# Optimization experiments

Hardware: AMD Instinct MI355X
Metric: run time of the kernel (lower is better)

The kernel has to match this reference:

```python
import jax, jax.numpy as jnp
import numpy as np

ALPHA = 0.2          # LeakyReLU negative slope
NEG_INF = -9e15      # mask value used by the torch module


def setup_inputs() -> dict:
    key = jax.random.key(0)
    k1, k2, k3, k4 = jax.random.split(key, 4)
    N, F_IN, F_OUT = 8192, 128, 128
    h = jax.random.normal(k1, (N, F_IN), dtype=jnp.float32)
    adj = jax.random.randint(k2, (N, N), 0, 2, dtype=jnp.int32)
    # xavier_uniform(gain=1.414) approximated with scaled normal init
    W = jax.random.normal(k3, (F_IN, F_OUT), dtype=jnp.float32) * (1.414 / np.sqrt(F_IN))
    a = jax.random.normal(k4, (2 * F_OUT, 1), dtype=jnp.float32) * (1.414 / np.sqrt(2 * F_OUT))
    return {"h": h, "adj": adj, "W": W, "a": a}


def reference(h, adj, W, a):
    # Wh: [N, F]
    Wh = h @ W
    F_out = W.shape[1]
    # e[i,j] = LeakyReLU( [Wh_i || Wh_j] . a ) = LeakyReLU( Wh_i.a1 + Wh_j.a2 )
    e_src = Wh @ a[:F_out, 0]   # [N]
    e_dst = Wh @ a[F_out:, 0]   # [N]
    e = jax.nn.leaky_relu(e_src[:, None] + e_dst[None, :], negative_slope=ALPHA)  # [N, N]
    attention = jax.nn.softmax(jnp.where(adj > 0, e, NEG_INF), axis=1)
    # dropout is identity in eval mode
    h_prime = attention @ Wh    # [N, F]
    return h_prime
```

## Files before the change

kernel.cpp:

```cpp
#include <hip/hip_runtime.h>
#include <hip/hip_bf16.h>


#define NN 8192
#define FF 128
#define SEGS 8
#define JSEG (NN / SEGS)
#define NK (JSEG / 32)

typedef __bf16 bf16x8 __attribute__((ext_vector_type(8)));
typedef float floatx4 __attribute__((ext_vector_type(4)));

__device__ __forceinline__ unsigned short f2b(float f) {
    unsigned int u = __float_as_uint(f);
    return (unsigned short)((u + 0x7FFFu + ((u >> 16) & 1u)) >> 16);
}
__device__ __forceinline__ unsigned int pk2(float a, float b) {
    return (unsigned int)f2b(a) | ((unsigned int)f2b(b) << 16);
}

__global__ __launch_bounds__(128) void k0_uv(const float* __restrict__ W,
                                             const float* __restrict__ a,
                                             float* __restrict__ u,
                                             float* __restrict__ v) {
    int k = blockIdx.x, t = threadIdx.x;
    float wv = W[k * FF + t];
    float p1 = wv * a[t];
    float p2 = wv * a[FF + t];
    for (int off = 32; off; off >>= 1) {
        p1 += __shfl_down(p1, off);
        p2 += __shfl_down(p2, off);
    }
    __shared__ float r[4];
    if ((t & 63) == 0) { r[(t >> 6) * 2] = p1; r[(t >> 6) * 2 + 1] = p2; }
    __syncthreads();
    if (t == 0) { u[k] = r[0] + r[2]; v[k] = r[1] + r[3]; }
}

__global__ __launch_bounds__(256) void k1_wh(const float* __restrict__ h,
                                             const float* __restrict__ W,
                                             const float* __restrict__ u,
                                             const float* __restrict__ v,
                                             unsigned short* __restrict__ WhT,
                                             float* __restrict__ e_src,
                                             float* __restrict__ e_dst) {
    __shared__ float hL[32 * 132];
    __shared__ float wL[128 * 132];
    __shared__ float uL[128], vL[128];
    __shared__ unsigned short tL[128 * 40];

    int t = threadIdx.x;
    int i0 = blockIdx.x * 32;

    {
        int row = t >> 3, c = (t & 7) * 16;
        const float4* s = (const float4*)&h[(i0 + row) * FF + c];
        float4* d = (float4*)&hL[row * 132 + c];
        #pragma unroll
        for (int j = 0; j < 4; j++) d[j] = s[j];
    }
    {
        int row = t >> 1, c = (t & 1) * 64;
        const float4* s = (const float4*)&W[row * FF + c];
        float4* d = (float4*)&wL[row * 132 + c];
        #pragma unroll
        for (int j = 0; j < 16; j++) d[j] = s[j];
    }
    if (t < 128) { uL[t] = u[t]; vL[t] = v[t]; }
    __syncthreads();

    int r0 = (t & 7) * 4;
    int c0 = (t >> 3) * 4;
    float acc[4][4] = {};
    for (int k0 = 0; k0 < 128; k0 += 4) {
        float4 hr[4], wr[4];
        #pragma unroll
        for (int i = 0; i < 4; i++) hr[i] = *(const float4*)&hL[(r0 + i) * 132 + k0];
        #pragma unroll
        for (int i = 0; i < 4; i++) wr[i] = *(const float4*)&wL[(k0 + i) * 132 + c0];
        #pragma unroll
        for (int kj = 0; kj < 4; kj++) {
            #pragma unroll
            for (int ri = 0; ri < 4; ri++) {
                float hvv = ((const float*)&hr[ri])[kj];
                const float* wvv = (const float*)&wr[kj];
                #pragma unroll
                for (int cj = 0; cj < 4; cj++) acc[ri][cj] = fmaf(hvv, wvv[cj], acc[ri][cj]);
            }
        }
    }
    #pragma unroll
    for (int ri = 0; ri < 4; ri++)
        #pragma unroll
        for (int cj = 0; cj < 4; cj++)
            tL[(c0 + cj) * 40 + r0 + ri] = f2b(acc[ri][cj]);
    __syncthreads();

    if (t < 64) {
        int row = t & 31;
        const float* sv = (t < 32) ? uL : vL;
        float s = 0.f;
        for (int k = 0; k < 128; k += 4) {
            float4 h4 = *(const float4*)&hL[row * 132 + k];
            float4 s4 = *(const float4*)&sv[k];
            s = fmaf(h4.x, s4.x, s); s = fmaf(h4.y, s4.y, s);
            s = fmaf(h4.z, s4.z, s); s = fmaf(h4.w, s4.w, s);
        }
        (t < 32 ? e_src : e_dst)[i0 + row] = s;
    }
    {
        int f = t & 127, half = t >> 7;
        const uint4* s = (const uint4*)&tL[f * 40 + half * 16];
        uint4* d = (uint4*)&WhT[f * NN + i0 + half * 16];
        d[0] = s[0]; d[1] = s[1];
    }
}

__device__ __forceinline__ float mask_w(int a, float x) {
    float l = fmaxf(x, 0.2f * x);
    return a > 0 ? __expf(l) : 0.f;
}

__global__ __launch_bounds__(512, 4) void k2_gat(const int* __restrict__ adj,
                                                 const unsigned short* __restrict__ WhT,
                                                 const float* __restrict__ e_src,
                                                 const float* __restrict__ e_dst,
                                                 float* __restrict__ num_ws,
                                                 float* __restrict__ den_ws) {
    int t = threadIdx.x;
    int bx = blockIdx.x;
    int it = bx >> 3, seg = bx & 7;
    int i0 = it * 128;
    int jb = seg * JSEG;

    int lane = t & 63, wave = t >> 6;
    int mrow = lane & 15, quad = lane >> 4;
    int irow = i0 + wave * 16 + mrow;

    float es = e_src[irow];
    const int*   Ap = adj + (size_t)irow * NN + jb + quad * 8;
    const float* Ep = e_dst + jb + quad * 8;

    const unsigned short* Bp[8];
    #pragma unroll
    for (int bn = 0; bn < 8; bn++)
        Bp[bn] = WhT + (size_t)(bn * 16 + mrow) * NN + jb + quad * 8;

    floatx4 acc[8] = {};
    float dsum = 0.f;

    int4   a0 = *(const int4*)Ap;
    int4   a1 = *(const int4*)(Ap + 4);
    float4 e0 = *(const float4*)Ep;
    float4 e1 = *(const float4*)(Ep + 4);

    for (int ks = 0; ks < NK; ks++) {
        bf16x8 B[8];
        #pragma unroll
        for (int bn = 0; bn < 8; bn++)
            B[bn] = *(const bf16x8*)(Bp[bn] + ks * 32);

        int nxt = (ks + 1 < NK ? ks + 1 : ks) * 32;
        int4   na0 = *(const int4*)(Ap + nxt);
        int4   na1 = *(const int4*)(Ap + nxt + 4);
        float4 ne0 = *(const float4*)(Ep + nxt);
        float4 ne1 = *(const float4*)(Ep + nxt + 4);

        float w0 = mask_w(a0.x, es + e0.x);
        float w1 = mask_w(a0.y, es + e0.y);
        float w2 = mask_w(a0.z, es + e0.z);
        float w3 = mask_w(a0.w, es + e0.w);
        float w4 = mask_w(a1.x, es + e1.x);
        float w5 = mask_w(a1.y, es + e1.y);
        float w6 = mask_w(a1.z, es + e1.z);
        float w7 = mask_w(a1.w, es + e1.w);
        dsum += ((w0 + w1) + (w2 + w3)) + ((w4 + w5) + (w6 + w7));

        union { unsigned int u[4]; bf16x8 v; } af;
        af.u[0] = pk2(w0, w1);
        af.u[1] = pk2(w2, w3);
        af.u[2] = pk2(w4, w5);
        af.u[3] = pk2(w6, w7);
        bf16x8 A = af.v;

        #pragma unroll
        for (int bn = 0; bn < 8; bn++)
            acc[bn] = __builtin_amdgcn_mfma_f32_16x16x32_bf16(A, B[bn], acc[bn], 0, 0, 0);

        a0 = na0; a1 = na1; e0 = ne0; e1 = ne1;
    }

    dsum += __shfl_xor(dsum, 16);
    dsum += __shfl_xor(dsum, 32);
    if (quad == 0) den_ws[seg * NN + irow] = dsum;

    float* np = num_ws + (size_t)seg * NN * FF;
    #pragma unroll
    for (int bn = 0; bn < 8; bn++)
        #pragma unroll
        for (int r = 0; r < 4; r++) {
            int row = i0 + wave * 16 + quad * 4 + r;
            np[(size_t)row * FF + bn * 16 + mrow] = acc[bn][r];
        }
}

__global__ __launch_bounds__(256) void k3_merge(const float* __restrict__ num_ws,
                                                const float* __restrict__ den_ws,
                                                float* __restrict__ out) {
    int idx = blockIdx.x * 256 + threadIdx.x;
    int i = idx >> 5;
    int c = (idx & 31) << 2;
    float4 s = make_float4(0.f, 0.f, 0.f, 0.f);
    float d = 0.f;
    #pragma unroll
    for (int sg = 0; sg < SEGS; sg++) {
        float4 vv = *(const float4*)&num_ws[(size_t)sg * NN * FF + (size_t)i * FF + c];
        s.x += vv.x; s.y += vv.y; s.z += vv.z; s.w += vv.w;
        d += den_ws[sg * NN + i];
    }
    float r = 1.0f / d;
    s.x *= r; s.y *= r; s.z *= r; s.w *= r;
    *(float4*)&out[(size_t)i * FF + c] = s;
}

extern "C" void kernel_launch(void* const* d_in, const int* in_sizes, int n_in,
                              void* d_out, int out_size, void* d_ws, size_t ws_size,
                              hipStream_t stream) {
    const float* h   = (const float*)d_in[0];
    const int*   adj = (const int*)d_in[1];
    const float* W   = (const float*)d_in[2];
    const float* a   = (const float*)d_in[3];
    float* out = (float*)d_out;

    char* ws = (char*)d_ws;
    unsigned short* WhT = (unsigned short*)ws;
    float* u     = (float*)(ws + 2097152);
    float* v     = u + 128;
    float* e_src = (float*)(ws + 2097152 + 1024);
    float* e_dst = e_src + NN;
    float* num_ws = (float*)(ws + 4194304);
    float* den_ws = (float*)(ws + 4194304 + 33554432);

    k0_uv<<<dim3(128), dim3(128), 0, stream>>>(W, a, u, v);
    k1_wh<<<dim3(256), dim3(256), 0, stream>>>(h, W, u, v, WhT, e_src, e_dst);
    k2_gat<<<dim3((NN / 128) * SEGS), dim3(512), 0, stream>>>(adj, WhT, e_src, e_dst, num_ws, den_ws);
    k3_merge<<<dim3(NN * FF / 4 / 256), dim3(256), 0, stream>>>(num_ws, den_ws, out);
}
```

Before: 483.2 us.

## Pack adjacency into bitmask, retile WhT, and double rows per wave in GAT kernel

Adds a pre-pass kernel that compresses the int32 adjacency matrix into a per-row bitmask, so the main attention kernel reads bits instead of 32-bit ints. WhT is stored in 32-column tiles, which makes the B-fragment loads contiguous. Each wave now handles two 16-row groups that share the B loads, with 256-thread blocks. The j dimension is split into 16 segments instead of 8. The full 256MB adjacency read still happens once in the pre-pass, and the larger num workspace doubles the merge traffic.

```diff
diff --git a/kernel.cpp b/kernel.cpp
--- a/kernel.cpp
+++ b/kernel.cpp
@@ -4,9 +4,8 @@
 
 #define NN 8192
 #define FF 128
-#define SEGS 8
+#define SEGS 16
 #define JSEG (NN / SEGS)
-#define NK (JSEG / 32)
 
 typedef __bf16 bf16x8 __attribute__((ext_vector_type(8)));
 typedef float floatx4 __attribute__((ext_vector_type(4)));
@@ -41,7 +40,7 @@
                                              const float* __restrict__ W,
                                              const float* __restrict__ u,
                                              const float* __restrict__ v,
-                                             unsigned short* __restrict__ WhT,
+                                             unsigned short* __restrict__ WhT2,
                                              float* __restrict__ e_src,
                                              float* __restrict__ e_dst) {
     __shared__ float hL[32 * 132];
@@ -111,102 +110,154 @@
     {
         int f = t & 127, half = t >> 7;
         const uint4* s = (const uint4*)&tL[f * 40 + half * 16];
-        uint4* d = (uint4*)&WhT[f * NN + i0 + half * 16];
+        uint4* d = (uint4*)&WhT2[(size_t)blockIdx.x * 4096 + f * 32 + half * 16];
         d[0] = s[0]; d[1] = s[1];
     }
 }
 
-__device__ __forceinline__ float mask_w(int a, float x) {
+__global__ __launch_bounds__(256) void k1b_bits(const int* __restrict__ adj,
+                                                unsigned char* __restrict__ bits) {
+    int row = blockIdx.x;
+    int t = threadIdx.x;
+    int lane = t & 63, wave = t >> 6;
+    const int* Ap = adj + (size_t)row * NN;
+    #pragma unroll
+    for (int i = 0; i < 4; i++) {
+        int col = wave * 2048 + i * 512 + lane * 8;
+        int4 a0 = *(const int4*)(Ap + col);
+        int4 a1 = *(const int4*)(Ap + col + 4);
+        unsigned int b =
+            (a0.x > 0 ? 1u : 0u)  | (a0.y > 0 ? 2u : 0u) |
+            (a0.z > 0 ? 4u : 0u)  | (a0.w > 0 ? 8u : 0u) |
+            (a1.x > 0 ? 16u : 0u) | (a1.y > 0 ? 32u : 0u) |
+            (a1.z > 0 ? 64u : 0u) | (a1.w > 0 ? 128u : 0u);
+        bits[(size_t)row * 1024 + (col >> 3)] = (unsigned char)b;
+    }
+}
+
+__device__ __forceinline__ float wfn(unsigned int bit, float x) {
     float l = fmaxf(x, 0.2f * x);
-    return a > 0 ? __expf(l) : 0.f;
-}
-
-__global__ __launch_bounds__(512, 4) void k2_gat(const int* __restrict__ adj,
-                                                 const unsigned short* __restrict__ WhT,
+    float e = __expf(l);
+    return bit ? e : 0.f;
+}
+
+__global__ __launch_bounds__(256, 4) void k2_gat(const unsigned int* __restrict__ bits,
+                                                 const unsigned short* __restrict__ WhT2,
                                                  const float* __restrict__ e_src,
                                                  const float* __restrict__ e_dst,
                                                  float* __restrict__ num_ws,
                                                  float* __restrict__ den_ws) {
     int t = threadIdx.x;
     int bx = blockIdx.x;
-    int it = bx >> 3, seg = bx & 7;
+    int it = bx >> 4, seg = bx & 15;
     int i0 = it * 128;
     int jb = seg * JSEG;
 
     int lane = t & 63, wave = t >> 6;
     int mrow = lane & 15, quad = lane >> 4;
-    int irow = i0 + wave * 16 + mrow;
-
-    float es = e_src[irow];
-    const int*   Ap = adj + (size_t)irow * NN + jb + quad * 8;
-    const float* Ep = e_dst + jb + quad * 8;
-
-    const unsigned short* Bp[8];
-    #pragma unroll
-    for (int bn = 0; bn < 8; bn++)
-        Bp[bn] = WhT + (size_t)(bn * 16 + mrow) * NN + jb + quad * 8;
-
-    floatx4 acc[8] = {};
-    float dsum = 0.f;
-
-    int4   a0 = *(const int4*)Ap;
-    int4   a1 = *(const int4*)(Ap + 4);
-    float4 e0 = *(const float4*)Ep;
-    float4 e1 = *(const float4*)(Ep + 4);
-
-    for (int ks = 0; ks < NK; ks++) {
-        bf16x8 B[8];
-        #pragma unroll
-        for (int bn = 0; bn < 8; bn++)
-            B[bn] = *(const bf16x8*)(Bp[bn] + ks * 32);
-
-        int nxt = (ks + 1 < NK ? ks + 1 : ks) * 32;
-        int4   na0 = *(const int4*)(Ap + nxt);
-        int4   na1 = *(const int4*)(Ap + nxt + 4);
-        float4 ne0 = *(const float4*)(Ep + nxt);
-        float4 ne1 = *(const float4*)(Ep + nxt + 4);
-
-        float w0 = mask_w(a0.x, es + e0.x);
-        float w1 = mask_w(a0.y, es + e0.y);
-        float w2 = mask_w(a0.z, es + e0.z);
-        float w3 = mask_w(a0.w, es + e0.w);
-        float w4 = mask_w(a1.x, es + e1.x);
-        float w5 = mask_w(a1.y, es + e1.y);
-        float w6 = mask_w(a1.z, es + e1.z);
-        float w7 = mask_w(a1.w, es + e1.w);
-        dsum += ((w0 + w1) + (w2 + w3)) + ((w4 + w5) + (w6 + w7));
-
-        union { unsigned int u[4]; bf16x8 v; } af;
-        af.u[0] = pk2(w0, w1);
-        af.u[1] = pk2(w2, w3);
-        af.u[2] = pk2(w4, w5);
-        af.u[3] = pk2(w6, w7);
-        bf16x8 A = af.v;
-
-        #pragma unroll
-        for (int bn = 0; bn < 8; bn++)
-            acc[bn] = __builtin_amdgcn_mfma_f32_16x16x32_bf16(A, B[bn], acc[bn], 0, 0, 0);
-
-        a0 = na0; a1 = na1; e0 = ne0; e1 = ne1;
-    }
-
-    dsum += __shfl_xor(dsum, 16);
-    dsum += __shfl_xor(dsum, 32);
-    if (quad == 0) den_ws[seg * NN + irow] = dsum;
+    int row0 = i0 + wave * 32 + mrow;
+    int row1 = row0 + 16;
+    int qs = quad * 8;
+
+    float es0 = e_src[row0];
+    float es1 = e_src[row1];
+    const unsigned int* bp0 = bits + (size_t)row0 * 256 + (jb >> 5);
+    const unsigned int* bp1 = bits + (size_t)row1 * 256 + (jb >> 5);
+    const unsigned short* Bp = WhT2 + (size_t)(jb >> 5) * 4096 + mrow * 32 + qs;
+    const float* Ep = e_dst + jb + qs;
+
+    floatx4 acc0[8] = {};
+    floatx4 acc1[8] = {};
+    float ds0 = 0.f, ds1 = 0.f;
+
+    for (int kg = 0; kg < 4; kg++) {
+        uint4 bm0 = *(const uint4*)(bp0 + kg * 4);
+        uint4 bm1 = *(const uint4*)(bp1 + kg * 4);
+        #pragma unroll
+        for (int kq = 0; kq < 4; kq++) {
+            int ks = kg * 4 + kq;
+            unsigned int byt0 = ((&bm0.x)[kq] >> qs) & 0xFFu;
+            unsigned int byt1 = ((&bm1.x)[kq] >> qs) & 0xFFu;
+            float4 e0 = *(const float4*)(Ep + ks * 32);
+            float4 e1 = *(const float4*)(Ep + ks * 32 + 4);
+
+            float w00 = wfn(byt0 & 1u,   es0 + e0.x);
+            float w01 = wfn(byt0 & 2u,   es0 + e0.y);
+            float w02 = wfn(byt0 & 4u,   es0 + e0.z);
+            float w03 = wfn(byt0 & 8u,   es0 + e0.w);
+            float w04 = wfn(byt0 & 16u,  es0 + e1.x);
+            float w05 = wfn(byt0 & 32u,  es0 + e1.y);
+            float w06 = wfn(byt0 & 64u,  es0 + e1.z);
+            float w07 = wfn(byt0 & 128u, es0 + e1.w);
+            float w10 = wfn(byt1 & 1u,   es1 + e0.x);
+            float w11 = wfn(byt1 & 2u,   es1 + e0.y);
+            float w12 = wfn(byt1 & 4u,   es1 + e0.z);
+            float w13 = wfn(byt1 & 8u,   es1 + e0.w);
+            float w14 = wfn(byt1 & 16u,  es1 + e1.x);
+            float w15 = wfn(byt1 & 32u,  es1 + e1.y);
+            float w16 = wfn(byt1 & 64u,  es1 + e1.z);
+            float w17 = wfn(byt1 & 128u, es1 + e1.w);
+
+            ds0 += ((w00 + w01) + (w02 + w03)) + ((w04 + w05) + (w06 + w07));
+            ds1 += ((w10 + w11) + (w12 + w13)) + ((w14 + w15) + (w16 + w17));
+
+            union { unsigned int u[4]; bf16x8 v; } A0, A1;
+            A0.u[0] = pk2(w00, w01); A0.u[1] = pk2(w02, w03);
+            A0.u[2] = pk2(w04, w05); A0.u[3] = pk2(w06, w07);
+            A1.u[0] = pk2(w10, w11); A1.u[1] = pk2(w12, w13);
+            A1.u[2] = pk2(w14, w15); A1.u[3] = pk2(w16, w17);
+
+            const unsigned short* pk = Bp + ks * 4096;
+            bf16x8 B0 = *(const bf16x8*)(pk);
+            bf16x8 B1 = *(const bf16x8*)(pk + 512);
+            bf16x8 B2 = *(const bf16x8*)(pk + 1024);
+            bf16x8 B3 = *(const bf16x8*)(pk + 1536);
+            acc0[0] = __builtin_amdgcn_mfma_f32_16x16x32_bf16(A0.v, B0, acc0[0], 0, 0, 0);
+            acc1[0] = __builtin_amdgcn_mfma_f32_16x16x32_bf16(A1.v, B0, acc1[0], 0, 0, 0);
+            acc0[1] = __builtin_amdgcn_mfma_f32_16x16x32_bf16(A0.v, B1, acc0[1], 0, 0, 0);
+            acc1[1] = __builtin_amdgcn_mfma_f32_16x16x32_bf16(A1.v, B1, acc1[1], 0, 0, 0);
+            acc0[2] = __builtin_amdgcn_mfma_f32_16x16x32_bf16(A0.v, B2, acc0[2], 0, 0, 0);
+            acc1[2] = __builtin_amdgcn_mfma_f32_16x16x32_bf16(A1.v, B2, acc1[2], 0, 0, 0);
+            acc0[3] = __builtin_amdgcn_mfma_f32_16x16x32_bf16(A0.v, B3, acc0[3], 0, 0, 0);
+            acc1[3] = __builtin_amdgcn_mfma_f32_16x16x32_bf16(A1.v, B3, acc1[3], 0, 0, 0);
+            bf16x8 B4 = *(const bf16x8*)(pk + 2048);
+            bf16x8 B5 = *(const bf16x8*)(pk + 2560);
+            bf16x8 B6 = *(const bf16x8*)(pk + 3072);
+            bf16x8 B7 = *(const bf16x8*)(pk + 3584);
+            acc0[4] = __builtin_amdgcn_mfma_f32_16x16x32_bf16(A0.v, B4, acc0[4], 0, 0, 0);
+            acc1[4] = __builtin_amdgcn_mfma_f32_16x16x32_bf16(A1.v, B4, acc1[4], 0, 0, 0);
+            acc0[5] = __builtin_amdgcn_mfma_f32_16x16x32_bf16(A0.v, B5, acc0[5], 0, 0, 0);
+            acc1[5] = __builtin_amdgcn_mfma_f32_16x16x32_bf16(A1.v, B5, acc1[5], 0, 0, 0);
+            acc0[6] = __builtin_amdgcn_mfma_f32_16x16x32_bf16(A0.v, B6, acc0[6], 0, 0, 0);
+            acc1[6] = __builtin_amdgcn_mfma_f32_16x16x32_bf16(A1.v, B6, acc1[6], 0, 0, 0);
+            acc0[7] = __builtin_amdgcn_mfma_f32_16x16x32_bf16(A0.v, B7, acc0[7], 0, 0, 0);
+            acc1[7] = __builtin_amdgcn_mfma_f32_16x16x32_bf16(A1.v, B7, acc1[7], 0, 0, 0);
+        }
+    }
+
+    ds0 += __shfl_xor(ds0, 16);
+    ds0 += __shfl_xor(ds0, 32);
+    ds1 += __shfl_xor(ds1, 16);
+    ds1 += __shfl_xor(ds1, 32);
+    if (quad == 0) {
+        den_ws[seg * NN + row0] = ds0;
+        den_ws[seg * NN + row1] = ds1;
+    }
 
     float* np = num_ws + (size_t)seg * NN * FF;
     #pragma unroll
     for (int bn = 0; bn < 8; bn++)
         #pragma unroll
         for (int r = 0; r < 4; r++) {
-            int row = i0 + wave * 16 + quad * 4 + r;
-            np[(size_t)row * FF + bn * 16 + mrow] = acc[bn][r];
+            int orow = i0 + wave * 32 + quad * 4 + r;
+            np[(size_t)orow * FF + bn * 16 + mrow] = acc0[bn][r];
+            np[(size_t)(orow + 16) * FF + bn * 16 + mrow] = acc1[bn][r];
         }
 }
 
 __global__ __launch_bounds__(256) void k3_merge(const float* __restrict__ num_ws,
-                                                const float* __restrict__ den_ws,
-                                                float* __restrict__ out) {
+                                               const float* __restrict__ den_ws,
+                                               float* __restrict__ out) {
     int idx = blockIdx.x * 256 + threadIdx.x;
     int i = idx >> 5;
     int c = (idx & 31) << 2;
@@ -233,16 +284,18 @@
     float* out = (float*)d_out;
 
     char* ws = (char*)d_ws;
-    unsigned short* WhT = (unsigned short*)ws;
+    unsigned short* WhT2 = (unsigned short*)ws;
     float* u     = (float*)(ws + 2097152);
     float* v     = u + 128;
     float* e_src = (float*)(ws + 2097152 + 1024);
     float* e_dst = e_src + NN;
-    float* num_ws = (float*)(ws + 4194304);
-    float* den_ws = (float*)(ws + 4194304 + 33554432);
+    unsigned char* bits = (unsigned char*)(ws + 3145728);
+    float* num_ws = (float*)(ws + 16777216);
+    float* den_ws = (float*)(ws + 16777216 + 67108864);
 
     k0_uv<<<dim3(128), dim3(128), 0, stream>>>(W, a, u, v);
-    k1_wh<<<dim3(256), dim3(256), 0, stream>>>(h, W, u, v, WhT, e_src, e_dst);
-    k2_gat<<<dim3((NN / 128) * SEGS), dim3(512), 0, stream>>>(adj, WhT, e_src, e_dst, num_ws, den_ws);
+    k1_wh<<<dim3(256), dim3(256), 0, stream>>>(h, W, u, v, WhT2, e_src, e_dst);
+    k1b_bits<<<dim3(NN), dim3(256), 0, stream>>>(adj, bits);
+    k2_gat<<<dim3((NN / 128) * SEGS), dim3(256), 0, stream>>>((const unsigned int*)bits, WhT2, e_src, e_dst, num_ws, den_ws);
     k3_merge<<<dim3(NN * FF / 4 / 256), dim3(256), 0, stream>>>(num_ws, den_ws, out);
 }
```

Result: slower. 524.6 us (+8.6%).
